# Performance work log

Hardware: AMD Instinct MI355X
Metric: run time of the kernel (lower is better)

## Reference

```python
import jax, jax.numpy as jnp
import numpy as np
from jax import lax

B, S, C = 32, 512, 32          # batch, seq_len (words), char_len
V, E = 101, 64                 # char vocab (printable + pad), emb size
F, K = 128, 3                  # n_filters, kernel_size


def setup_inputs() -> dict:
    key = jax.random.key(0)
    k0, k1, k2, k3 = jax.random.split(key, 4)
    char_ids = jax.random.randint(k0, (B, S, C), 0, V, dtype=jnp.int32)
    emb_table = jax.random.normal(k1, (V, E), dtype=jnp.float32)
    emb_table = emb_table.at[0].set(0.0)  # padding_idx=0
    fan_in = E * K
    conv_w = jax.random.normal(k2, (F, E, K), dtype=jnp.float32) / np.sqrt(fan_in)
    conv_b = jax.random.normal(k3, (F,), dtype=jnp.float32) * 0.01
    return {"char_ids": char_ids, "emb_table": emb_table,
            "conv_w": conv_w, "conv_b": conv_b}


def reference(char_ids, emb_table, conv_w, conv_b):
    b, s, c = char_ids.shape
    e = emb_table.shape[1]
    # embedding lookup: [B, S, C, E]; dropout p=0.0 (eval) -> identity
    char_embs = emb_table[char_ids]
    # FAITHFUL to torch source: .view(-1, E, C) is a raw row-major
    # reinterpretation of the contiguous [B*S, C, E] buffer (not a permute).
    x = char_embs.reshape(b * s, e, c)  # [B*S, E, C] by memory layout
    # Conv1d over the last axis, valid padding
    y = lax.conv_general_dilated(
        x, conv_w, window_strides=(1,), padding="VALID",
        dimension_numbers=("NCH", "OIH", "NCH"))  # [B*S, F, C-K+1]
    y = y + conv_b[None, :, None]
    # max-pool over time, then back to [B, S, F]
    return y.max(axis=2).reshape(b, s, -1)
```

## Files before the change

### kernel.cpp

```cpp
#include <hip/hip_runtime.h>
#include <cstdint>


typedef __bf16 bf16x8 __attribute__((ext_vector_type(8)));
typedef float  f32x16 __attribute__((ext_vector_type(16)));

#define GW   4
#define NGRP 4
#define ROWS 34
#define RST  72

__global__ __launch_bounds__(256)
void prep_pack_w(const float* __restrict__ w, __bf16* __restrict__ pw) {
  int i = blockIdx.x * 256 + threadIdx.x;
  int j    = i & 7;
  int lane = (i >> 3) & 63;
  int ks   = (i >> 9) & 3;
  int t    = i >> 11;
  int kk   = t % 3;
  int nt   = t / 3;
  int f = nt * 32 + (lane & 31);
  int e = ks * 16 + (lane >> 5) * 8 + j;
  pw[i] = (__bf16)w[f * 192 + e * 3 + kk];
}

__global__ __launch_bounds__(256, 4)
void charcnn_mfma(const int* __restrict__ cid, const float* __restrict__ emb,
                  const float* __restrict__ bias, const __bf16* __restrict__ pw,
                  float* __restrict__ out) {
  __shared__ __align__(16) __bf16 xT[8][ROWS * RST];

  const int tid  = threadIdx.x;
  const int lane = tid & 63;
  const int wv   = tid >> 6;

  bf16x8 bfrag[12];
  const bf16x8* pwv = (const bf16x8*)pw;
#pragma unroll
  for (int q = 0; q < 12; ++q)
    bfrag[q] = pwv[(wv * 12 + q) * 64 + lane];

  const float vb = bias[wv * 32 + (lane & 31)];

  const int a  = tid >> 3;
  const int p  = tid & 7;
  const int d0 = p * 4;
  const int bw = blockIdx.x * (GW * NGRP);

  auto stage_group = [&](int g) {
    const int w0 = g * GW;
    int ch[GW];
#pragma unroll
    for (int i = 0; i < GW; ++i)
      ch[i] = cid[(bw + w0 + i) * 32 + a];
#pragma unroll
    for (int i = 0; i < GW; ++i) {
      const float4* er = (const float4*)(emb + ch[i] * 64);
      float4 lo = er[p];
      float4 hi = er[p + 8];
      uint32_t* dst = (uint32_t*)(&xT[(w0 + i) & 7][0]);
      float lv[4] = {lo.x, lo.y, lo.z, lo.w};
      float hv[4] = {hi.x, hi.y, hi.z, hi.w};
#pragma unroll
      for (int i2 = 0; i2 < 4; ++i2) {
        uint32_t u = ((uint32_t)__builtin_bit_cast(uint16_t, (__bf16)hv[i2]) << 16)
                   |  (uint32_t)__builtin_bit_cast(uint16_t, (__bf16)lv[i2]);
        dst[(d0 + i2) * 36 + a] = u;
      }
    }
  };

  auto compute_word = [&](int w) {
    const __bf16* xb = &xT[w & 7][0];
    f32x16 acc;
#pragma unroll
    for (int i2 = 0; i2 < 16; ++i2) acc[i2] = 0.0f;

#pragma unroll
    for (int kk = 0; kk < 3; ++kk) {
#pragma unroll
      for (int ks = 0; ks < 4; ++ks) {
        const bf16x8* ap = (const bf16x8*)(xb + ((lane & 31) + kk) * RST
                                              + ks * 16 + (lane >> 5) * 8);
        acc = __builtin_amdgcn_mfma_f32_32x32x16_bf16(*ap, bfrag[kk * 4 + ks],
                                                      acc, 0, 0, 0);
      }
    }

    float m0 = acc[0];
#pragma unroll
    for (int r = 1; r <= 13; ++r) m0 = fmaxf(m0, acc[r]);
    float m1 = fmaxf(acc[14], acc[15]);
    float mm = (lane < 32) ? fmaxf(m0, m1) : m0;
    float other = __shfl_xor(mm, 32, 64);
    float fullmax = fmaxf(mm, other) + vb;
    if (lane < 32) out[(bw + w) * 128 + wv * 32 + lane] = fullmax;
  };

  stage_group(0);
  __syncthreads();

  for (int g = 0; g < NGRP; ++g) {
    if (g + 1 < NGRP) stage_group(g + 1);
    const int w0 = g * GW;
#pragma unroll
    for (int i = 0; i < GW; ++i) compute_word(w0 + i);
    __syncthreads();
  }
}

extern "C" void kernel_launch(void* const* d_in, const int* in_sizes, int n_in,
                              void* d_out, int out_size, void* d_ws, size_t ws_size,
                              hipStream_t stream) {
  const int*   cid = (const int*)d_in[0];
  const float* emb = (const float*)d_in[1];
  const float* cw  = (const float*)d_in[2];
  const float* cb  = (const float*)d_in[3];
  float* outp = (float*)d_out;
  __bf16* pw = (__bf16*)d_ws;

  hipLaunchKernelGGL(prep_pack_w, dim3(96), dim3(256), 0, stream, cw, pw);
  hipLaunchKernelGGL(charcnn_mfma, dim3(1024), dim3(256), 0, stream,
                     cid, emb, cb, (const __bf16*)pw, outp);
}
```

Baseline: 35.71 us.

## Split waves across words and filter pairs, prefetch char ids and software-pipeline staging

Each wave now computes two 32-filter tiles for half the words instead of one tile for all words, so every LDS A-fragment load feeds two MFMAs and LDS read traffic per MFMA is halved. All char ids are loaded up front, and the embedding gather is split into a global-load phase before compute and an LDS-write phase after it, so load latency can overlap the MFMA work. The cost is twice the B-fragment registers, and the launch bound drops from 4 to 2 blocks per SM, which may reduce occupancy. The max reduction becomes a tree, and the trailing sync is dropped.

```diff
diff --git a/kernel.cpp b/kernel.cpp
--- a/kernel.cpp
+++ b/kernel.cpp
@@ -7,6 +7,7 @@
 
 #define GW   4
 #define NGRP 4
+#define NW   16
 #define ROWS 34
 #define RST  72
 
@@ -24,7 +25,7 @@
   pw[i] = (__bf16)w[f * 192 + e * 3 + kk];
 }
 
-__global__ __launch_bounds__(256, 4)
+__global__ __launch_bounds__(256, 2)
 void charcnn_mfma(const int* __restrict__ cid, const float* __restrict__ emb,
                   const float* __restrict__ bias, const __bf16* __restrict__ pw,
                   float* __restrict__ out) {
@@ -33,34 +34,47 @@
   const int tid  = threadIdx.x;
   const int lane = tid & 63;
   const int wv   = tid >> 6;
+  const int np   = wv & 1;
+  const int ws   = wv >> 1;
 
-  bf16x8 bfrag[12];
+  bf16x8 bfrag[2][12];
   const bf16x8* pwv = (const bf16x8*)pw;
 #pragma unroll
-  for (int q = 0; q < 12; ++q)
-    bfrag[q] = pwv[(wv * 12 + q) * 64 + lane];
+  for (int nt = 0; nt < 2; ++nt)
+#pragma unroll
+    for (int q = 0; q < 12; ++q)
+      bfrag[nt][q] = pwv[((np * 2 + nt) * 12 + q) * 64 + lane];
 
-  const float vb = bias[wv * 32 + (lane & 31)];
+  const float vb0 = bias[(np * 2 + 0) * 32 + (lane & 31)];
+  const float vb1 = bias[(np * 2 + 1) * 32 + (lane & 31)];
 
   const int a  = tid >> 3;
   const int p  = tid & 7;
   const int d0 = p * 4;
-  const int bw = blockIdx.x * (GW * NGRP);
+  const int bw = blockIdx.x * NW;
 
-  auto stage_group = [&](int g) {
-    const int w0 = g * GW;
-    int ch[GW];
+  int chw[NW];
 #pragma unroll
-    for (int i = 0; i < GW; ++i)
-      ch[i] = cid[(bw + w0 + i) * 32 + a];
+  for (int w = 0; w < NW; ++w) chw[w] = cid[(bw + w) * 32 + a];
+
+  float4 slo[GW], shi[GW];
+
+  auto stage_load = [&](int g) {
 #pragma unroll
     for (int i = 0; i < GW; ++i) {
-      const float4* er = (const float4*)(emb + ch[i] * 64);
-      float4 lo = er[p];
-      float4 hi = er[p + 8];
+      const float4* er = (const float4*)(emb + chw[g * GW + i] * 64);
+      slo[i] = er[p];
+      shi[i] = er[p + 8];
+    }
+  };
+
+  auto stage_write = [&](int g) {
+    const int w0 = g * GW;
+#pragma unroll
+    for (int i = 0; i < GW; ++i) {
       uint32_t* dst = (uint32_t*)(&xT[(w0 + i) & 7][0]);
-      float lv[4] = {lo.x, lo.y, lo.z, lo.w};
-      float hv[4] = {hi.x, hi.y, hi.z, hi.w};
+      float lv[4] = {slo[i].x, slo[i].y, slo[i].z, slo[i].w};
+      float hv[4] = {shi[i].x, shi[i].y, shi[i].z, shi[i].w};
 #pragma unroll
       for (int i2 = 0; i2 < 4; ++i2) {
         uint32_t u = ((uint32_t)__builtin_bit_cast(uint16_t, (__bf16)hv[i2]) << 16)
@@ -70,42 +84,57 @@
     }
   };
 
+  auto finish = [&](const f32x16& acc, float vbv, int fcol, int w) {
+    float m01 = fmaxf(acc[0],  acc[1]);
+    float m23 = fmaxf(acc[2],  acc[3]);
+    float m45 = fmaxf(acc[4],  acc[5]);
+    float m67 = fmaxf(acc[6],  acc[7]);
+    float m89 = fmaxf(acc[8],  acc[9]);
+    float mab = fmaxf(acc[10], acc[11]);
+    float mcd = fmaxf(acc[12], acc[13]);
+    float q0 = fmaxf(m01, m23);
+    float q1 = fmaxf(m45, m67);
+    float q2 = fmaxf(m89, mab);
+    float m0 = fmaxf(fmaxf(q0, q1), fmaxf(q2, mcd));
+    float m1 = fmaxf(acc[14], acc[15]);
+    float mm = (lane < 32) ? fmaxf(m0, m1) : m0;
+    float other = __shfl_xor(mm, 32, 64);
+    float fullmax = fmaxf(mm, other) + vbv;
+    if (lane < 32) out[(bw + w) * 128 + fcol + lane] = fullmax;
+  };
+
   auto compute_word = [&](int w) {
-    const __bf16* xb = &xT[w & 7][0];
-    f32x16 acc;
+    const __bf16* xb = &xT[w & 7][0] + (lane & 31) * RST + (lane >> 5) * 8;
+    f32x16 acc0, acc1;
 #pragma unroll
-    for (int i2 = 0; i2 < 16; ++i2) acc[i2] = 0.0f;
+    for (int r = 0; r < 16; ++r) { acc0[r] = 0.0f; acc1[r] = 0.0f; }
 
 #pragma unroll
     for (int kk = 0; kk < 3; ++kk) {
 #pragma unroll
       for (int ks = 0; ks < 4; ++ks) {
-        const bf16x8* ap = (const bf16x8*)(xb + ((lane & 31) + kk) * RST
-                                              + ks * 16 + (lane >> 5) * 8);
-        acc = __builtin_amdgcn_mfma_f32_32x32x16_bf16(*ap, bfrag[kk * 4 + ks],
-                                                      acc, 0, 0, 0);
+        bf16x8 av = *(const bf16x8*)(xb + kk * RST + ks * 16);
+        acc0 = __builtin_amdgcn_mfma_f32_32x32x16_bf16(av, bfrag[0][kk * 4 + ks],
+                                                       acc0, 0, 0, 0);
+        acc1 = __builtin_amdgcn_mfma_f32_32x32x16_bf16(av, bfrag[1][kk * 4 + ks],
+                                                       acc1, 0, 0, 0);
       }
     }
-
-    float m0 = acc[0];
-#pragma unroll
-    for (int r = 1; r <= 13; ++r) m0 = fmaxf(m0, acc[r]);
-    float m1 = fmaxf(acc[14], acc[15]);
-    float mm = (lane < 32) ? fmaxf(m0, m1) : m0;
-    float other = __shfl_xor(mm, 32, 64);
-    float fullmax = fmaxf(mm, other) + vb;
-    if (lane < 32) out[(bw + w) * 128 + wv * 32 + lane] = fullmax;
+    finish(acc0, vb0, np * 64,      w);
+    finish(acc1, vb1, np * 64 + 32, w);
   };
 
-  stage_group(0);
+  stage_load(0);
+  stage_write(0);
   __syncthreads();
 
+#pragma unroll
   for (int g = 0; g < NGRP; ++g) {
-    if (g + 1 < NGRP) stage_group(g + 1);
-    const int w0 = g * GW;
-#pragma unroll
-    for (int i = 0; i < GW; ++i) compute_word(w0 + i);
-    __syncthreads();
+    if (g + 1 < NGRP) stage_load(g + 1);
+    compute_word(g * GW + ws);
+    compute_word(g * GW + ws + 2);
+    if (g + 1 < NGRP) stage_write(g + 1);
+    if (g + 1 < NGRP) __syncthreads();
   }
 }
 
```

After: 35.10 us. About the same (-1.7%).
